# Performance work log

Hardware: AMD Instinct MI355X
Metric: run time of the kernel (lower is better)

The kernel has to match this reference:

```python
import jax, jax.numpy as jnp
import numpy as np

V, D, L, H, FF, MAXLEN = 32000, 512, 6, 8, 2048, 4096
B, S = 8, 1024
DH = D // H
EPS = 1e-5


def _pos_encoding(max_len, d_model):
    pos = np.arange(max_len)[:, None].astype(np.float32)
    div = np.exp(np.arange(0, d_model, 2).astype(np.float32) * (-np.log(10000.0) / d_model))
    pe = np.zeros((max_len, d_model), dtype=np.float32)
    pe[:, 0::2] = np.sin(pos * div)
    pe[:, 1::2] = np.cos(pos * div)
    return jnp.asarray(pe)


def setup_inputs() -> dict:
    key = jax.random.key(0)
    ks = jax.random.split(key, 16)
    s = 0.02
    inp = {
        'src': jax.random.randint(ks[0], (B, S), 0, V),
        'mask': jnp.ones((B, 1, 1, S), dtype=jnp.int32),
        'emb': s * jax.random.normal(ks[1], (V, D), dtype=jnp.float32),
        'pe': _pos_encoding(MAXLEN, D),
        # stacked per-layer params [L, ...]; Linear stored as [d_in, d_out]
        'wq': s * jax.random.normal(ks[2], (L, D, D), dtype=jnp.float32),
        'bq': jnp.zeros((L, D), dtype=jnp.float32),
        'wk': s * jax.random.normal(ks[3], (L, D, D), dtype=jnp.float32),
        'bk': jnp.zeros((L, D), dtype=jnp.float32),
        'wv': s * jax.random.normal(ks[4], (L, D, D), dtype=jnp.float32),
        'bv': jnp.zeros((L, D), dtype=jnp.float32),
        'wo': s * jax.random.normal(ks[5], (L, D, D), dtype=jnp.float32),
        'bo': jnp.zeros((L, D), dtype=jnp.float32),
        'w1': s * jax.random.normal(ks[6], (L, D, FF), dtype=jnp.float32),
        'b1': jnp.zeros((L, FF), dtype=jnp.float32),
        'w2': s * jax.random.normal(ks[7], (L, FF, D), dtype=jnp.float32),
        'b2': jnp.zeros((L, D), dtype=jnp.float32),
        'g1': jnp.ones((L, D), dtype=jnp.float32),
        'be1': jnp.zeros((L, D), dtype=jnp.float32),
        'g2': jnp.ones((L, D), dtype=jnp.float32),
        'be2': jnp.zeros((L, D), dtype=jnp.float32),
    }
    return inp


def _layernorm(x, g, b):
    mu = jnp.mean(x, axis=-1, keepdims=True)
    var = jnp.mean(jnp.square(x - mu), axis=-1, keepdims=True)
    return (x - mu) * jax.lax.rsqrt(var + EPS) * g + b


def _encoder(src, mask, emb, pe, wq, bq, wk, bk, wv, bv, wo, bo,
             w1, b1, w2, b2, g1, be1, g2, be2):
    b, s = src.shape
    x = emb[src] + pe[None, :s, :]  # [B,S,D]; dropout is identity (eval)

    def layer(x, p):
        (wq, bq, wk, bk, wv, bv, wo, bo, w1, b1, w2, b2, g1, be1, g2, be2) = p
        def heads(y):
            return y.reshape(b, s, H, DH).transpose(0, 2, 1, 3)  # [B,H,S,Dh]
        Q = heads(x @ wq + bq)
        K = heads(x @ wk + bk)
        Vv = heads(x @ wv + bv)
        scores = jnp.einsum('bhqd,bhkd->bhqk', Q, K) / jnp.sqrt(jnp.float32(DH))
        scores = jnp.where(mask == 0, -jnp.inf, scores)
        attn = jax.nn.softmax(scores, axis=-1)
        out = jnp.einsum('bhqk,bhkd->bhqd', attn, Vv)
        out = out.transpose(0, 2, 1, 3).reshape(b, s, D) @ wo + bo
        x1 = _layernorm(x + out, g1, be1)
        ff = jax.nn.relu(x1 @ w1 + b1) @ w2 + b2
        return _layernorm(x1 + ff, g2, be2), None

    params = (wq, bq, wk, bk, wv, bv, wo, bo, w1, b1, w2, b2, g1, be1, g2, be2)
    x, _ = jax.lax.scan(layer, x, params)
    return x


def reference(src, mask, emb, pe, wq, bq, wk, bk, wv, bv, wo, bo,
              w1, b1, w2, b2, g1, be1, g2, be2):
    return _encoder(src, mask, emb, pe, wq, bq, wk, bk, wv, bv, wo, bo,
                    w1, b1, w2, b2, g1, be1, g2, be2)
```

## Files before the change

### kernel.cpp

```cpp
#include <hip/hip_runtime.h>
#include <stdint.h>

#define DEV static __device__ __forceinline__

typedef float f32x4 __attribute__((ext_vector_type(4)));
typedef short s16x8 __attribute__((ext_vector_type(8)));
typedef unsigned short u16;

constexpr int D   = 512;
constexpr int H   = 8;
constexpr int DHd = 64;
constexpr int S   = 1024;
constexpr int Bn  = 8;
constexpr int L   = 6;
constexpr int FF  = 2048;
constexpr int TOK = Bn * S;
constexpr int QKV = 3 * D;
constexpr int KVB = 64;

DEV u16 f2bf(float f) {
  union { float f; uint32_t u; } v; v.f = f;
  uint32_t u = v.u;
  u += 0x7FFFu + ((u >> 16) & 1u);
  return (u16)(u >> 16);
}

DEV uint32_t cvtpk(float a, float b) {
  uint32_t r;
  asm("v_cvt_pk_bf16_f32 %0, %1, %2" : "=v"(r) : "v"(a), "v"(b));
  return r;
}

DEV float bf2f(u16 u) {
  union { uint32_t u; float f; } t;
  t.u = ((uint32_t)u) << 16;
  return t.f;
}

DEV f32x4 mfma16(s16x8 a, s16x8 b, f32x4 c) {
  return __builtin_amdgcn_mfma_f32_16x16x32_bf16(a, b, c, 0, 0, 0);
}

typedef __attribute__((address_space(1))) const void GV;
typedef __attribute__((address_space(3))) void LV;
DEV void gload_lds16(const u16* g, u16* l) {
  __builtin_amdgcn_global_load_lds((GV*)g, (LV*)l, 16, 0, 0);
}

__global__ __launch_bounds__(256) void wprep4_kernel(const float* __restrict__ wq,
                                                     const float* __restrict__ wk,
                                                     const float* __restrict__ wv,
                                                     const float* __restrict__ wo,
                                                     u16* __restrict__ wqkvT,
                                                     u16* __restrict__ woT) {
  __shared__ float tile[32][33];
  const int z = blockIdx.z, which = z & 3, lyr = z >> 2;
  const float* in = (which == 0 ? wq : which == 1 ? wk : which == 2 ? wv : wo)
                    + (size_t)lyr * D * D;
  u16* out = (which < 3) ? wqkvT + (size_t)lyr * QKV * D + (size_t)which * D * D
                         : woT + (size_t)lyr * D * D;
  const int k0 = blockIdx.x * 32, n0 = blockIdx.y * 32;
  const int tx = (int)threadIdx.x & 31, ty = (int)threadIdx.x >> 5;
#pragma unroll
  for (int i = 0; i < 32; i += 8)
    tile[ty + i][tx] = in[(size_t)(k0 + ty + i) * D + n0 + tx];
  __syncthreads();
#pragma unroll
  for (int i = 0; i < 32; i += 8)
    out[(size_t)(n0 + ty + i) * D + k0 + tx] = f2bf(tile[tx][ty + i]);
}

__global__ __launch_bounds__(256) void wprep_kernel(const float* __restrict__ in,
                                                    u16* __restrict__ out, int K, int N,
                                                    size_t ostride) {
  __shared__ float tile[32][33];
  const int zl = blockIdx.z;
  in  += (size_t)zl * K * N;
  out += (size_t)zl * ostride;
  const int k0 = blockIdx.x * 32, n0 = blockIdx.y * 32;
  const int tx = (int)threadIdx.x & 31, ty = (int)threadIdx.x >> 5;
#pragma unroll
  for (int i = 0; i < 32; i += 8)
    tile[ty + i][tx] = in[(size_t)(k0 + ty + i) * N + n0 + tx];
  __syncthreads();
#pragma unroll
  for (int i = 0; i < 32; i += 8)
    out[(size_t)(n0 + ty + i) * K + k0 + tx] = f2bf(tile[tx][ty + i]);
}

__global__ __launch_bounds__(256) void prep_kernel(const float* __restrict__ bq,
                                                   const float* __restrict__ bk,
                                                   const float* __restrict__ bv,
                                                   const int* __restrict__ mask,
                                                   float* __restrict__ bqkv,
                                                   float* __restrict__ mb,
                                                   int* __restrict__ flags) {
  const int blk = (int)blockIdx.x;
  const int tid = (int)threadIdx.x;
  if (blk < 36) {
    const int i = blk * 256 + tid;
    const int l = i / QKV, r = i % QKV;
    const float* src = (r < D) ? bq : (r < 2 * D ? bk : bv);
    bqkv[i] = src[l * D + (r & (D - 1))];
  } else if (blk < 68) {
    const int i = (blk - 36) * 256 + tid;
    mb[i] = (mask[i] == 0) ? -3e38f : 0.f;
  } else if (tid < 128) {
    const int* m = mask + (tid >> 4) * S + (tid & 15) * 64;
    int all = 1;
#pragma unroll
    for (int j = 0; j < 64; ++j) all &= (m[j] != 0) ? 1 : 0;
    flags[tid] = all;
  }
}

__global__ __launch_bounds__(256) void embed_kernel(const int* __restrict__ src,
                                                    const float* __restrict__ emb,
                                                    const float* __restrict__ pe,
                                                    u16* __restrict__ xb) {
  const int t = blockIdx.x;
  const int s = t & (S - 1);
  const int tok = src[t];
  const int c = (int)threadIdx.x * 2;
  const float* ep = emb + (size_t)tok * D + c;
  const float* pp = pe + (size_t)s * D + c;
  *(uint32_t*)(xb + (size_t)t * D + c) = cvtpk(ep[0] + pp[0], ep[1] + pp[1]);
}

template <int MT, int VMODE, int KSPLIT>
__global__ __launch_bounds__(256) void gemm_kernel(const u16* __restrict__ A,
                                                   const u16* __restrict__ BT,
                                                   const float* __restrict__ bias,
                                                   u16* __restrict__ outB,
                                                   u16* __restrict__ outV,
                                                   int N, int K, int relu) {
  constexpr int BM = MT * 32;
  constexpr float QSCL = 0.125f * 1.44269504089f;
  __shared__ u16 sA[BM * 64];
  __shared__ u16 sB[128 * 64];
  const int tid = (int)threadIdx.x;
  const int w = tid >> 6, l = tid & 63;
  const int wr = w >> 1, wc = w & 1;
  const int lr = l & 15, lg = l >> 4;

  const int nwg = (int)gridDim.x;
  const int bid = (int)blockIdx.x;
  const int wg  = (bid & 7) * (nwg >> 3) + (bid >> 3);
  const int nbn = N >> 7;
  int kidx = 0, rem = wg;
  if constexpr (KSPLIT > 1) {
    const int per = nwg / KSPLIT;
    kidx = wg / per;
    rem  = wg % per;
  }
  const int bm = (rem / nbn) * BM, bn = (rem % nbn) * 128;
  const int KS = K / KSPLIT;

  f32x4 acc[MT][4];
#pragma unroll
  for (int i = 0; i < MT; ++i)
#pragma unroll
    for (int j = 0; j < 4; ++j)
#pragma unroll
      for (int r = 0; r < 4; ++r) acc[i][j][r] = 0.f;

  const int srow = tid >> 3;
  const int scol = (tid & 7) * 8;
  const u16* Ag = A + (size_t)(bm + srow) * K + kidx * KS + scol;
  const u16* Bg = BT + (size_t)(bn + srow) * K + kidx * KS + scol;
  u16* sAd = sA + srow * 64 + scol;
  u16* sBd = sB + srow * 64 + scol;

  for (int kt = 0; kt < KS; kt += 64) {
    __syncthreads();
#pragma unroll
    for (int r = 0; r < BM / 32; ++r)
      gload_lds16(Ag + (size_t)(r * 32) * K + kt, sAd + r * 32 * 64);
#pragma unroll
    for (int r = 0; r < 4; ++r)
      gload_lds16(Bg + (size_t)(r * 32) * K + kt, sBd + r * 32 * 64);
    __syncthreads();
#pragma unroll
    for (int kk = 0; kk < 2; ++kk) {
      s16x8 af[MT], bfr[4];
#pragma unroll
      for (int mt = 0; mt < MT; ++mt)
        af[mt] = *(const s16x8*)&sA[(wr * MT * 16 + mt * 16 + lr) * 64 + kk * 32 + lg * 8];
#pragma unroll
      for (int nt = 0; nt < 4; ++nt)
        bfr[nt] = *(const s16x8*)&sB[(wc * 64 + nt * 16 + lr) * 64 + kk * 32 + lg * 8];
#pragma unroll
      for (int mt = 0; mt < MT; ++mt)
#pragma unroll
        for (int nt = 0; nt < 4; ++nt)
          acc[mt][nt] = mfma16(af[mt], bfr[nt], acc[mt][nt]);
    }
  }

#pragma unroll
  for (int mt = 0; mt < MT; ++mt)
#pragma unroll
    for (int nt = 0; nt < 4; ++nt) {
      const int col = bn + wc * 64 + nt * 16 + lr;
      const int row0 = bm + wr * MT * 16 + mt * 16 + lg * 4;
      if constexpr (KSPLIT > 1) {
        u16* op = outB + (size_t)kidx * TOK * N + (size_t)row0 * N + col;
        const uint32_t p01 = cvtpk(acc[mt][nt][0], acc[mt][nt][1]);
        const uint32_t p23 = cvtpk(acc[mt][nt][2], acc[mt][nt][3]);
        op[0]               = (u16)p01;
        op[N]               = (u16)(p01 >> 16);
        op[2 * (size_t)N]   = (u16)p23;
        op[3 * (size_t)N]   = (u16)(p23 >> 16);
      } else {
        const float bv = bias ? bias[col] : 0.f;
        if (VMODE && col >= 2 * D) {
          const int dcol = col - 2 * D;
          const int hh = dcol >> 6, dh = dcol & 63;
          const int bb = row0 >> 10, s = row0 & (S - 1);
          u16* vp = outV + ((size_t)((bb << 3) + hh) * DHd + dh) * S + s;
          *(uint32_t*)(vp)     = cvtpk(acc[mt][nt][0] + bv, acc[mt][nt][1] + bv);
          *(uint32_t*)(vp + 2) = cvtpk(acc[mt][nt][2] + bv, acc[mt][nt][3] + bv);
        } else {
          float v[4];
#pragma unroll
          for (int r = 0; r < 4; ++r) {
            v[r] = acc[mt][nt][r] + bv;
            if (relu) v[r] = fmaxf(v[r], 0.f);
            if (VMODE && col < D) v[r] *= QSCL;
          }
          const size_t o0 = (size_t)row0 * N + col;
          const uint32_t p01 = cvtpk(v[0], v[1]);
          const uint32_t p23 = cvtpk(v[2], v[3]);
          outB[o0]                   = (u16)p01;
          outB[o0 + N]               = (u16)(p01 >> 16);
          outB[o0 + 2 * (size_t)N]   = (u16)p23;
          outB[o0 + 3 * (size_t)N]   = (u16)(p23 >> 16);
        }
      }
    }
}

__global__ __launch_bounds__(512) void attn_kernel(const u16* __restrict__ qkv,
                                                   const u16* __restrict__ vt,
                                                   const int* __restrict__ mflags,
                                                   const float* __restrict__ mb,
                                                   u16* __restrict__ attno) {
  __shared__ u16 sK[2][KVB * 72];
  __shared__ u16 sV[2][KVB * 72];
  __shared__ u16 sP[8][16][72];
  const int tid = (int)threadIdx.x;
  const int w = tid >> 6, l = tid & 63;
  const int lr = l & 15, lg = l >> 4;
  const int bid = (int)blockIdx.x;
  const int wg  = (bid & 7) * 32 + (bid >> 3);
  const int bh = wg >> 2, qc = wg & 3;
  const int b = bh >> 3, h = bh & 7;
  const int q0 = qc * 256 + w * 32;

  const u16* qr0 = qkv + (size_t)(b * S + q0 + lr) * QKV + h * DHd;
  const u16* qr1 = qr0 + (size_t)16 * QKV;
  const s16x8 aq0 = *(const s16x8*)(qr0 + lg * 8);
  const s16x8 aq1 = *(const s16x8*)(qr0 + 32 + lg * 8);
  const s16x8 aq2 = *(const s16x8*)(qr1 + lg * 8);
  const s16x8 aq3 = *(const s16x8*)(qr1 + 32 + lg * 8);
  const u16* kbase = qkv + D + (size_t)b * S * QKV + h * DHd;
  const u16* vbase = vt + (size_t)bh * DHd * S;
  const float* mrow0 = mb + b * S;

  s16x8 vones;
#pragma unroll
  for (int i = 0; i < 8; ++i) vones[i] = (short)0x3F80;

  const int srow = tid >> 3;
  const int sc16 = tid & 7;
  const u16* kg = kbase + (size_t)srow * QKV + sc16 * 8;
  const u16* vg = vbase + (size_t)srow * S + sc16 * 8;
  const int soff = srow * 72 + sc16 * 8;

  uint4 ka = *(const uint4*)kg;
  uint4 va = *(const uint4*)vg;
  *(uint4*)&sK[0][soff] = ka;
  *(uint4*)&sV[0][soff] = va;
  ka = *(const uint4*)(kg + (size_t)KVB * QKV);
  va = *(const uint4*)(vg + KVB);
  __syncthreads();

  f32x4 o[2][4], osum[2];
#pragma unroll
  for (int f = 0; f < 2; ++f) {
#pragma unroll
    for (int nt = 0; nt < 4; ++nt)
#pragma unroll
      for (int r = 0; r < 4; ++r) o[f][nt][r] = 0.f;
#pragma unroll
    for (int r = 0; r < 4; ++r) osum[f][r] = 0.f;
  }

  constexpr int NTILE = S / KVB;
  for (int t = 0; t < NTILE; ++t) {
    const int cur = t & 1;
    if (t + 1 < NTILE) {
      *(uint4*)&sK[cur ^ 1][soff] = ka;
      *(uint4*)&sV[cur ^ 1][soff] = va;
    }
    if (t + 2 < NTILE) {
      ka = *(const uint4*)(kg + (size_t)(t + 2) * KVB * QKV);
      va = *(const uint4*)(vg + (t + 2) * KVB);
    }

    f32x4 sa[2][4];
#pragma unroll
    for (int kt = 0; kt < 4; ++kt) {
      const u16* kr = &sK[cur][(kt * 16 + lr) * 72];
      const s16x8 bk0 = *(const s16x8*)(kr + lg * 8);
      const s16x8 bk1 = *(const s16x8*)(kr + 32 + lg * 8);
      f32x4 za, zb;
#pragma unroll
      for (int r = 0; r < 4; ++r) { za[r] = 0.f; zb[r] = 0.f; }
      za = mfma16(bk0, aq0, za);
      sa[0][kt] = mfma16(bk1, aq1, za);
      zb = mfma16(bk0, aq2, zb);
      sa[1][kt] = mfma16(bk1, aq3, zb);
    }

    if (!mflags[(b << 4) + t]) {
#pragma unroll
      for (int kt = 0; kt < 4; ++kt) {
        const f32x4 mk = *(const f32x4*)(mrow0 + t * KVB + kt * 16 + lg * 4);
#pragma unroll
        for (int r = 0; r < 4; ++r) {
          sa[0][kt][r] += mk[r];
          sa[1][kt][r] += mk[r];
        }
      }
    }

#pragma unroll
    for (int f = 0; f < 2; ++f)
#pragma unroll
      for (int kt = 0; kt < 4; ++kt)
#pragma unroll
        for (int r = 0; r < 4; ++r) sa[f][kt][r] = exp2f(sa[f][kt][r]);

    s16x8 bv[2][4];
#pragma unroll
    for (int ks = 0; ks < 2; ++ks)
#pragma unroll
      for (int nt = 0; nt < 4; ++nt)
        bv[ks][nt] = *(const s16x8*)&sV[cur][(nt * 16 + lr) * 72 + ks * 32 + lg * 8];

#pragma unroll
    for (int f = 0; f < 2; ++f) {
#pragma unroll
      for (int kt = 0; kt < 4; ++kt) {
        uint2 pk;
        pk.x = cvtpk(sa[f][kt][0], sa[f][kt][1]);
        pk.y = cvtpk(sa[f][kt][2], sa[f][kt][3]);
        *(uint2*)&sP[w][lr][kt * 16 + lg * 4] = pk;
      }
#pragma unroll
      for (int ks = 0; ks < 2; ++ks) {
        const s16x8 ap = *(const s16x8*)&sP[w][lr][ks * 32 + lg * 8];
        osum[f] = mfma16(ap, vones, osum[f]);
#pragma unroll
        for (int nt = 0; nt < 4; ++nt)
          o[f][nt] = mfma16(ap, bv[ks][nt], o[f][nt]);
      }
    }
    __syncthreads();
  }

#pragma unroll
  for (int f = 0; f < 2; ++f) {
    float li[4];
#pragma unroll
    for (int r = 0; r < 4; ++r) li[r] = 1.f / osum[f][r];
#pragma unroll
    for (int nt = 0; nt < 4; ++nt) {
      u16* op = attno + (size_t)(b * S + q0 + f * 16 + lg * 4) * D + h * DHd + nt * 16 + lr;
#pragma unroll
      for (int r = 0; r < 4; r += 2) {
        const uint32_t pk = cvtpk(o[f][nt][r] * li[r], o[f][nt][r + 1] * li[r + 1]);
        op[(size_t)r * D]       = (u16)pk;
        op[(size_t)(r + 1) * D] = (u16)(pk >> 16);
      }
    }
  }
}

template <int NP>
__global__ __launch_bounds__(256) void ln_kernel(const u16* __restrict__ p,
                                                 const float* __restrict__ bias,
                                                 const u16* __restrict__ resid,
                                                 const float* __restrict__ g,
                                                 const float* __restrict__ be,
                                                 float* __restrict__ outf,
                                                 u16* __restrict__ outb) {
  const int w = (int)threadIdx.x >> 6, l = (int)threadIdx.x & 63;
  const int t = (int)blockIdx.x * 4 + w;
  const size_t base = (size_t)t * D + l * 8;
  f32x4 v0 = *(const f32x4*)(bias + l * 8);
  f32x4 v1 = *(const f32x4*)(bias + l * 8 + 4);
  {
    const s16x8 rv = *(const s16x8*)(resid + base);
#pragma unroll
    for (int i = 0; i < 4; ++i) {
      v0[i] += bf2f((u16)rv[i]);
      v1[i] += bf2f((u16)rv[i + 4]);
    }
  }
#pragma unroll
  for (int np = 0; np < NP; ++np) {
    const s16x8 pv = *(const s16x8*)(p + (size_t)np * TOK * D + base);
#pragma unroll
    for (int i = 0; i < 4; ++i) {
      v0[i] += bf2f((u16)pv[i]);
      v1[i] += bf2f((u16)pv[i + 4]);
    }
  }
  float s = 0.f, sq = 0.f;
#pragma unroll
  for (int i = 0; i < 4; ++i) {
    s += v0[i] + v1[i];
    sq += v0[i] * v0[i] + v1[i] * v1[i];
  }
  for (int m = 1; m < 64; m <<= 1) {
    s += __shfl_xor(s, m);
    sq += __shfl_xor(sq, m);
  }
  const float mu = s * (1.0f / D);
  const float var = sq * (1.0f / D) - mu * mu;
  const float rs = rsqrtf(var + 1e-5f);
  const f32x4 g0 = *(const f32x4*)(g + l * 8);
  const f32x4 g1v = *(const f32x4*)(g + l * 8 + 4);
  const f32x4 b0 = *(const f32x4*)(be + l * 8);
  const f32x4 b1v = *(const f32x4*)(be + l * 8 + 4);
  f32x4 y0, y1;
#pragma unroll
  for (int i = 0; i < 4; ++i) {
    y0[i] = (v0[i] - mu) * rs * g0[i] + b0[i];
    y1[i] = (v1[i] - mu) * rs * g1v[i] + b1v[i];
  }
  uint4 ob;
  ob.x = cvtpk(y0[0], y0[1]);
  ob.y = cvtpk(y0[2], y0[3]);
  ob.z = cvtpk(y1[0], y1[1]);
  ob.w = cvtpk(y1[2], y1[3]);
  if (outf) {
    *(f32x4*)(outf + base) = y0;
    *(f32x4*)(outf + base + 4) = y1;
  }
  *(uint4*)(outb + base) = ob;
}

extern "C" void kernel_launch(void* const* d_in, const int* in_sizes, int n_in,
                              void* d_out, int out_size, void* d_ws, size_t ws_size,
                              hipStream_t stream) {
  (void)in_sizes; (void)n_in; (void)out_size; (void)ws_size;
  const int*   src  = (const int*)d_in[0];
  const int*   mask = (const int*)d_in[1];
  const float* emb  = (const float*)d_in[2];
  const float* pe   = (const float*)d_in[3];
  const float* wq = (const float*)d_in[4];  const float* bq = (const float*)d_in[5];
  const float* wk = (const float*)d_in[6];  const float* bk = (const float*)d_in[7];
  const float* wv = (const float*)d_in[8];  const float* bv = (const float*)d_in[9];
  const float* wo = (const float*)d_in[10]; const float* bo = (const float*)d_in[11];
  const float* w1 = (const float*)d_in[12]; const float* b1 = (const float*)d_in[13];
  const float* w2 = (const float*)d_in[14]; const float* b2 = (const float*)d_in[15];
  const float* g1 = (const float*)d_in[16]; const float* be1 = (const float*)d_in[17];
  const float* g2 = (const float*)d_in[18]; const float* be2 = (const float*)d_in[19];

  char* ws = (char*)d_ws;
  size_t off = 0;
  auto alloc = [&](size_t bytes) -> void* {
    void* p = ws + off;
    off += (bytes + 255) & ~(size_t)255;
    return p;
  };

  u16* wqkvT = (u16*)alloc((size_t)L * QKV * D * 2);
  u16* woT   = (u16*)alloc((size_t)L * D * D * 2);
  u16* w1T   = (u16*)alloc((size_t)L * D * FF * 2);
  u16* w2T   = (u16*)alloc((size_t)L * D * FF * 2);
  float* bqkv = (float*)alloc((size_t)L * QKV * 4);
  float* mbf  = (float*)alloc((size_t)TOK * 4);
  int*   mflg = (int*)alloc(128 * 4);
  u16* xb    = (u16*)alloc((size_t)TOK * D * 2);
  u16* x1b   = (u16*)alloc((size_t)TOK * D * 2);
  u16* attno = (u16*)alloc((size_t)TOK * D * 2);
  u16* qkvb  = (u16*)alloc((size_t)TOK * FF * 2);
  u16* vtb   = (u16*)alloc((size_t)TOK * D * 2);
  u16* hbuf  = qkvb;
  u16* pf    = (u16*)alloc((size_t)2 * TOK * D * 2);
  u16* po    = pf;

  const dim3 blk(256);

  wprep4_kernel<<<dim3(16, 16, 4 * L), blk, 0, stream>>>(wq, wk, wv, wo, wqkvT, woT);
  wprep_kernel<<<dim3(16, 64, L), blk, 0, stream>>>(w1, w1T, D, FF, (size_t)D * FF);
  wprep_kernel<<<dim3(64, 16, L), blk, 0, stream>>>(w2, w2T, FF, D, (size_t)D * FF);
  prep_kernel<<<dim3(69), blk, 0, stream>>>(bq, bk, bv, mask, bqkv, mbf, mflg);

  embed_kernel<<<TOK, blk, 0, stream>>>(src, emb, pe, xb);

  for (int lyr = 0; lyr < L; ++lyr) {
    const size_t wOffQ = (size_t)lyr * QKV * D;
    const size_t wOffD = (size_t)lyr * D * D;
    const size_t wOffF = (size_t)lyr * D * FF;
    gemm_kernel<2, 1, 1><<<dim3(128 * 12), blk, 0, stream>>>(xb, wqkvT + wOffQ, bqkv + lyr * QKV,
                                                             qkvb, vtb, QKV, D, 0);
    attn_kernel<<<dim3(256), dim3(512), 0, stream>>>(qkvb, vtb, mflg, mbf, attno);
    gemm_kernel<2, 0, 2><<<dim3(128 * 4 * 2), blk, 0, stream>>>(attno, woT + wOffD, nullptr,
                                                                po, nullptr, D, D, 0);
    ln_kernel<2><<<TOK / 4, blk, 0, stream>>>(po, bo + lyr * D, xb,
                                              g1 + lyr * D, be1 + lyr * D, nullptr, x1b);
    gemm_kernel<2, 0, 1><<<dim3(128 * 16), blk, 0, stream>>>(x1b, w1T + wOffF, b1 + lyr * FF,
                                                             hbuf, nullptr, FF, D, 1);
    gemm_kernel<2, 0, 2><<<dim3(128 * 4 * 2), blk, 0, stream>>>(hbuf, w2T + wOffF, nullptr,
                                                                pf, nullptr, D, FF, 0);
    float* xdst = (lyr == L - 1) ? (float*)d_out : nullptr;
    ln_kernel<2><<<TOK / 4, blk, 0, stream>>>(pf, b2 + lyr * D, x1b,
                                              g2 + lyr * D, be2 + lyr * D, xdst, xb);
  }
}
```

Measured before the change: 881.5 us.

## Swizzle GEMM LDS tiles, split attention P buffer per fragment, vectorize embed

GEMM tiles are now staged into shared memory with an XOR swizzle on the 8-element column chunks, so the MFMA fragment reads are meant to avoid LDS bank conflicts. The attention kernel gives each query fragment its own P buffer, so both fragments' probabilities are written before the PV MFMAs. This lets the two fragments' MFMAs interleave and removes the write-read serialization on one buffer, at the cost of more LDS. The embedding kernel handles 4 tokens per block with 8-wide vector loads and 16-byte stores, cutting the number of blocks and memory instructions.

```diff
diff --git a/kernel.cpp b/kernel.cpp
--- a/kernel.cpp
+++ b/kernel.cpp
@@ -118,13 +118,20 @@
                                                     const float* __restrict__ emb,
                                                     const float* __restrict__ pe,
                                                     u16* __restrict__ xb) {
-  const int t = blockIdx.x;
+  const int t = (int)blockIdx.x * 4 + ((int)threadIdx.x >> 6);
+  const int c = ((int)threadIdx.x & 63) * 8;
   const int s = t & (S - 1);
   const int tok = src[t];
-  const int c = (int)threadIdx.x * 2;
   const float* ep = emb + (size_t)tok * D + c;
   const float* pp = pe + (size_t)s * D + c;
-  *(uint32_t*)(xb + (size_t)t * D + c) = cvtpk(ep[0] + pp[0], ep[1] + pp[1]);
+  const f32x4 e0 = *(const f32x4*)ep,       e1 = *(const f32x4*)(ep + 4);
+  const f32x4 p0 = *(const f32x4*)pp,       p1 = *(const f32x4*)(pp + 4);
+  uint4 ob;
+  ob.x = cvtpk(e0[0] + p0[0], e0[1] + p0[1]);
+  ob.y = cvtpk(e0[2] + p0[2], e0[3] + p0[3]);
+  ob.z = cvtpk(e1[0] + p1[0], e1[1] + p1[1]);
+  ob.w = cvtpk(e1[2] + p1[2], e1[3] + p1[3]);
+  *(uint4*)(xb + (size_t)t * D + c) = ob;
 }
 
 template <int MT, int VMODE, int KSPLIT>
@@ -165,11 +172,12 @@
       for (int r = 0; r < 4; ++r) acc[i][j][r] = 0.f;
 
   const int srow = tid >> 3;
-  const int scol = (tid & 7) * 8;
-  const u16* Ag = A + (size_t)(bm + srow) * K + kidx * KS + scol;
-  const u16* Bg = BT + (size_t)(bn + srow) * K + kidx * KS + scol;
-  u16* sAd = sA + srow * 64 + scol;
-  u16* sBd = sB + srow * 64 + scol;
+  const int sswz = ((tid & 7) ^ (srow & 7)) * 8;
+  const int sdst = (tid & 7) * 8;
+  const u16* Ag = A + (size_t)(bm + srow) * K + kidx * KS + sswz;
+  const u16* Bg = BT + (size_t)(bn + srow) * K + kidx * KS + sswz;
+  u16* sAd = sA + srow * 64 + sdst;
+  u16* sBd = sB + srow * 64 + sdst;
 
   for (int kt = 0; kt < KS; kt += 64) {
     __syncthreads();
@@ -183,12 +191,13 @@
 #pragma unroll
     for (int kk = 0; kk < 2; ++kk) {
       s16x8 af[MT], bfr[4];
+      const int csw = ((kk * 4 + lg) ^ (lr & 7)) << 3;
 #pragma unroll
       for (int mt = 0; mt < MT; ++mt)
-        af[mt] = *(const s16x8*)&sA[(wr * MT * 16 + mt * 16 + lr) * 64 + kk * 32 + lg * 8];
+        af[mt] = *(const s16x8*)&sA[(wr * MT * 16 + mt * 16 + lr) * 64 + csw];
 #pragma unroll
       for (int nt = 0; nt < 4; ++nt)
-        bfr[nt] = *(const s16x8*)&sB[(wc * 64 + nt * 16 + lr) * 64 + kk * 32 + lg * 8];
+        bfr[nt] = *(const s16x8*)&sB[(wc * 64 + nt * 16 + lr) * 64 + csw];
 #pragma unroll
       for (int mt = 0; mt < MT; ++mt)
 #pragma unroll
@@ -247,7 +256,7 @@
                                                    u16* __restrict__ attno) {
   __shared__ u16 sK[2][KVB * 72];
   __shared__ u16 sV[2][KVB * 72];
-  __shared__ u16 sP[8][16][72];
+  __shared__ u16 sP[8][2][16][72];
   const int tid = (int)threadIdx.x;
   const int w = tid >> 6, l = tid & 63;
   const int lr = l & 15, lg = l >> 4;
@@ -342,29 +351,33 @@
 #pragma unroll
         for (int r = 0; r < 4; ++r) sa[f][kt][r] = exp2f(sa[f][kt][r]);
 
-    s16x8 bv[2][4];
-#pragma unroll
-    for (int ks = 0; ks < 2; ++ks)
-#pragma unroll
-      for (int nt = 0; nt < 4; ++nt)
-        bv[ks][nt] = *(const s16x8*)&sV[cur][(nt * 16 + lr) * 72 + ks * 32 + lg * 8];
-
-#pragma unroll
-    for (int f = 0; f < 2; ++f) {
+#pragma unroll
+    for (int f = 0; f < 2; ++f)
 #pragma unroll
       for (int kt = 0; kt < 4; ++kt) {
         uint2 pk;
         pk.x = cvtpk(sa[f][kt][0], sa[f][kt][1]);
         pk.y = cvtpk(sa[f][kt][2], sa[f][kt][3]);
-        *(uint2*)&sP[w][lr][kt * 16 + lg * 4] = pk;
+        *(uint2*)&sP[w][f][lr][kt * 16 + lg * 4] = pk;
       }
-#pragma unroll
-      for (int ks = 0; ks < 2; ++ks) {
-        const s16x8 ap = *(const s16x8*)&sP[w][lr][ks * 32 + lg * 8];
-        osum[f] = mfma16(ap, vones, osum[f]);
-#pragma unroll
-        for (int nt = 0; nt < 4; ++nt)
-          o[f][nt] = mfma16(ap, bv[ks][nt], o[f][nt]);
+
+    s16x8 bv[2][4];
+#pragma unroll
+    for (int ks = 0; ks < 2; ++ks)
+#pragma unroll
+      for (int nt = 0; nt < 4; ++nt)
+        bv[ks][nt] = *(const s16x8*)&sV[cur][(nt * 16 + lr) * 72 + ks * 32 + lg * 8];
+
+#pragma unroll
+    for (int ks = 0; ks < 2; ++ks) {
+      const s16x8 ap0 = *(const s16x8*)&sP[w][0][lr][ks * 32 + lg * 8];
+      const s16x8 ap1 = *(const s16x8*)&sP[w][1][lr][ks * 32 + lg * 8];
+      osum[0] = mfma16(ap0, vones, osum[0]);
+      osum[1] = mfma16(ap1, vones, osum[1]);
+#pragma unroll
+      for (int nt = 0; nt < 4; ++nt) {
+        o[0][nt] = mfma16(ap0, bv[ks][nt], o[0][nt]);
+        o[1][nt] = mfma16(ap1, bv[ks][nt], o[1][nt]);
       }
     }
     __syncthreads();
@@ -501,7 +514,7 @@
   wprep_kernel<<<dim3(64, 16, L), blk, 0, stream>>>(w2, w2T, FF, D, (size_t)D * FF);
   prep_kernel<<<dim3(69), blk, 0, stream>>>(bq, bk, bv, mask, bqkv, mbf, mflg);
 
-  embed_kernel<<<TOK, blk, 0, stream>>>(src, emb, pe, xb);
+  embed_kernel<<<TOK / 4, blk, 0, stream>>>(src, emb, pe, xb);
 
   for (int lyr = 0; lyr < L; ++lyr) {
     const size_t wOffQ = (size_t)lyr * QKV * D;
```

Result: faster. 828.1 us (median of 3 runs) (-6.1%).
